# Optimization experiments

Measured on AMD Instinct MI355X. Metric: run time of the kernel, lower is better.

## Reference

```python
import jax, jax.numpy as jnp
import numpy as np

D_MODEL = 1024
HEADS = 16
D_KEY = D_MODEL // HEADS


def setup_inputs() -> dict:
    key = jax.random.key(0)
    ks = jax.random.split(key, 7)
    B, S = 4, 2048
    queries = jax.random.normal(ks[0], (B, S, D_MODEL), dtype=jnp.float32)
    keys = jax.random.normal(ks[1], (B, S, D_MODEL), dtype=jnp.float32)
    values = jax.random.normal(ks[2], (B, S, D_MODEL), dtype=jnp.float32)
    scale = 1.0 / np.sqrt(D_MODEL)
    # Per-head projection weights, torch Linear layout [out=d_key, in=d_model], stacked over heads
    Wq = jax.random.uniform(ks[3], (HEADS, D_KEY, D_MODEL), jnp.float32, -scale, scale)
    Wk = jax.random.uniform(ks[4], (HEADS, D_KEY, D_MODEL), jnp.float32, -scale, scale)
    Wv = jax.random.uniform(ks[5], (HEADS, D_KEY, D_MODEL), jnp.float32, -scale, scale)
    Wo = jax.random.uniform(ks[6], (D_MODEL, D_MODEL), jnp.float32, -scale, scale)
    return {"queries": queries, "keys": keys, "values": values,
            "Wq": Wq, "Wk": Wk, "Wv": Wv, "Wo": Wo}


def reference(queries, keys, values, Wq, Wk, Wv, Wo):
    # Project per head: [B,S,D] x [H,K,D] -> [B,H,S,K]
    q = jnp.einsum('bsd,hkd->bhsk', queries, Wq)
    k = jnp.einsum('bsd,hkd->bhsk', keys, Wk)
    v = jnp.einsum('bsd,hkd->bhsk', values, Wv)
    attn = jnp.einsum('bhqk,bhsk->bhqs', q, k) / jnp.sqrt(jnp.float32(D_KEY))
    attn = jax.nn.softmax(attn, axis=-1)
    out = jnp.einsum('bhqs,bhsk->bhqk', attn, v)  # [B,H,S,K]
    B, H, S, K = out.shape
    # concat heads along last dim (head order = torch cat order)
    out = out.transpose(0, 2, 1, 3).reshape(B, S, H * K)
    return out @ Wo.T
```

## Files before the change

### kernel.cpp

```cpp
#include <hip/hip_runtime.h>
#include <hip/hip_bf16.h>

typedef __attribute__((ext_vector_type(8))) short short8;
typedef __attribute__((ext_vector_type(4))) short short4v;
typedef __attribute__((ext_vector_type(4))) float f32x4;
typedef __bf16 bf16x8 __attribute__((ext_vector_type(8)));
typedef __attribute__((ext_vector_type(2))) unsigned int u32x2;
typedef __attribute__((ext_vector_type(4))) unsigned int u32x4;

#define DEVI static __device__ __forceinline__

DEVI short f2bs(float f) {
    union { __hip_bfloat16 h; short s; } u;
    u.h = __float2bfloat16(f);
    return u.s;
}

DEVI unsigned pack2(float a, float b) {
    union { short s[2]; unsigned u; } u;
    u.s[0] = f2bs(a);
    u.s[1] = f2bs(b);
    return u.u;
}

DEVI void xchg(unsigned& x, unsigned& y) {
#if __has_builtin(__builtin_amdgcn_permlane32_swap) && __has_builtin(__builtin_amdgcn_permlane16_swap)
    u32x2 t = __builtin_amdgcn_permlane32_swap(x, y, false, false);
    u32x2 r = __builtin_amdgcn_permlane16_swap(t[0], t[1], false, false);
    x = r[0];
    y = r[1];
#else
    asm("v_permlane32_swap_b32 %0, %1" : "+v"(x), "+v"(y));
    asm("v_permlane16_swap_b32 %0, %1" : "+v"(x), "+v"(y));
#endif
}

DEVI f32x4 mfma16(short8 a, short8 b, f32x4 c) {
    return __builtin_amdgcn_mfma_f32_16x16x32_bf16(
        __builtin_bit_cast(bf16x8, a), __builtin_bit_cast(bf16x8, b), c, 0, 0, 0);
}

DEVI void glds16(const short* g, short* l) {
    __builtin_amdgcn_global_load_lds((const __attribute__((address_space(1))) void*)g,
                                     (__attribute__((address_space(3))) void*)l, 16, 0, 0);
}

__global__ __launch_bounds__(256) void cvt_all(const float4* __restrict__ q,
                                               const float4* __restrict__ k,
                                               const float4* __restrict__ v,
                                               const float4* __restrict__ wq,
                                               const float4* __restrict__ wk,
                                               const float4* __restrict__ wv,
                                               const float4* __restrict__ wo,
                                               short4v* __restrict__ dq,
                                               short4v* __restrict__ dk,
                                               short4v* __restrict__ dv,
                                               short4v* __restrict__ dwq,
                                               short4v* __restrict__ dwk,
                                               short4v* __restrict__ dwv,
                                               short4v* __restrict__ dwo) {
    int bid = blockIdx.x;
    float4 x;
    short4v s;
    if (bid < 8192) {
        int i = bid * 256 + threadIdx.x;
        x = q[i]; s.x = f2bs(x.x); s.y = f2bs(x.y); s.z = f2bs(x.z); s.w = f2bs(x.w); dq[i] = s;
        x = k[i]; s.x = f2bs(x.x); s.y = f2bs(x.y); s.z = f2bs(x.z); s.w = f2bs(x.w); dk[i] = s;
        x = v[i]; s.x = f2bs(x.x); s.y = f2bs(x.y); s.z = f2bs(x.z); s.w = f2bs(x.w); dv[i] = s;
    } else {
        int i = (bid - 8192) * 256 + threadIdx.x;
        x = wq[i]; s.x = f2bs(x.x); s.y = f2bs(x.y); s.z = f2bs(x.z); s.w = f2bs(x.w); dwq[i] = s;
        x = wk[i]; s.x = f2bs(x.x); s.y = f2bs(x.y); s.z = f2bs(x.z); s.w = f2bs(x.w); dwk[i] = s;
        x = wv[i]; s.x = f2bs(x.x); s.y = f2bs(x.y); s.z = f2bs(x.z); s.w = f2bs(x.w); dwv[i] = s;
        x = wo[i]; s.x = f2bs(x.x); s.y = f2bs(x.y); s.z = f2bs(x.z); s.w = f2bs(x.w); dwo[i] = s;
    }
}

template <typename EpiT>
DEVI void gemm_body(const short* A, const short* Bw, short* smem, int m0, int n0, EpiT epi) {
    short* As = smem;
    short* Bs = smem + 8192;
    const int t = threadIdx.x;
    const int lane = t & 63, w = t >> 6;
    const int col = lane & 15, quad = lane >> 4;
    const int wm = (w & 1) * 64, wn = (w >> 1) * 64;

    f32x4 acc[4][4];
#pragma unroll
    for (int i = 0; i < 4; ++i)
#pragma unroll
        for (int j = 0; j < 4; ++j) acc[i][j] = (f32x4){0.f, 0.f, 0.f, 0.f};

    for (int kt = 0; kt < 16; ++kt) {
        const int k0 = kt * 64;
#pragma unroll
        for (int j = 0; j < 4; ++j) {
            int cbase = (j * 4 + w) * 64;
            int c = cbase + lane;
            int row = c >> 3, kc = (c & 7) ^ (row & 7);
            glds16(A + (size_t)(m0 + row) * 1024 + k0 + kc * 8, As + cbase * 8);
        }
#pragma unroll
        for (int j = 0; j < 4; ++j) {
            int cbase = (j * 4 + w) * 64;
            int c = cbase + lane;
            int row = c >> 3, kc = (c & 7) ^ (row & 7);
            glds16(Bw + (size_t)(n0 + row) * 1024 + k0 + kc * 8, Bs + cbase * 8);
        }
        __syncthreads();
#pragma unroll
        for (int ks = 0; ks < 2; ++ks) {
            short8 a[4], b[4];
#pragma unroll
            for (int i = 0; i < 4; ++i) {
                int row = wm + i * 16 + col;
                int kc = (ks * 4 + quad) ^ (col & 7);
                a[i] = *(const short8*)(As + (row * 8 + kc) * 8);
            }
#pragma unroll
            for (int i = 0; i < 4; ++i) {
                int row = wn + i * 16 + col;
                int kc = (ks * 4 + quad) ^ (col & 7);
                b[i] = *(const short8*)(Bs + (row * 8 + kc) * 8);
            }
#pragma unroll
            for (int mi = 0; mi < 4; ++mi)
#pragma unroll
                for (int ni = 0; ni < 4; ++ni)
                    acc[mi][ni] = mfma16(a[mi], b[ni], acc[mi][ni]);
        }
        __syncthreads();
    }
    epi(acc, wm, wn, col, quad);
}

__global__ __launch_bounds__(256) void qkv_gemm(const short* __restrict__ xq,
                                                const short* __restrict__ xk,
                                                const short* __restrict__ xv,
                                                const short* __restrict__ wq,
                                                const short* __restrict__ wk,
                                                const short* __restrict__ wv,
                                                short* __restrict__ qp,
                                                short* __restrict__ kp,
                                                short* __restrict__ vpt, float qscale) {
    __shared__ __align__(16) short smem[17408];
    const int z = blockIdx.z;
    const int m0 = blockIdx.y * 128, n0 = blockIdx.x * 128;
    const short* A = (z == 0) ? xq : (z == 1) ? xk : xv;
    const short* W = (z == 0) ? wq : (z == 1) ? wk : wv;

    if (z < 2) {
        short* outs = (z == 0) ? qp : kp;
        const float scale = (z == 0) ? qscale : 1.0f;
        gemm_body(A, W, smem, m0, n0, [&](f32x4 (&acc)[4][4], int wm, int wn, int col, int quad) {
            short* T = smem;
#pragma unroll
            for (int mi = 0; mi < 4; ++mi)
#pragma unroll
                for (int ni = 0; ni < 4; ++ni)
#pragma unroll
                    for (int r = 0; r < 4; ++r)
                        T[(wm + mi * 16 + quad * 4 + r) * 136 + wn + ni * 16 + col] =
                            f2bs(acc[mi][ni][r] * scale);
            __syncthreads();
            int t = threadIdx.x;
            int ml = t >> 1, nh = (t & 1) * 64;
            int m = m0 + ml;
            int b = m >> 11, s = m & 2047;
#pragma unroll
            for (int j = 0; j < 8; ++j) {
                int n = n0 + nh + j * 8;
                short8 vv = *(const short8*)(T + ml * 136 + nh + j * 8);
                size_t off = ((size_t)(b * 16 + (n >> 6)) * 2048 + s) * 64 + (n & 63);
                *(short8*)(outs + off) = vv;
            }
        });
    } else {
        gemm_body(A, W, smem, m0, n0, [&](f32x4 (&acc)[4][4], int wm, int wn, int col, int quad) {
            short* T = smem;
#pragma unroll
            for (int mi = 0; mi < 4; ++mi)
#pragma unroll
                for (int ni = 0; ni < 4; ++ni) {
                    int n_l = wn + ni * 16 + col;
                    int m_l = wm + mi * 16 + quad * 4;
                    short4v sv;
                    sv.x = f2bs(acc[mi][ni][0]); sv.y = f2bs(acc[mi][ni][1]);
                    sv.z = f2bs(acc[mi][ni][2]); sv.w = f2bs(acc[mi][ni][3]);
                    *(short4v*)(T + n_l * 132 + m_l) = sv;
                }
            __syncthreads();
            int t = threadIdx.x;
            int nrow = t >> 1, mh = (t & 1) * 64;
            int b = m0 >> 11, s0 = m0 & 2047;
            size_t base = ((size_t)(b * 1024 + n0 + nrow)) * 2048 + s0 + mh;
#pragma unroll
            for (int j = 0; j < 16; ++j) {
                unsigned long long vv = *(const unsigned long long*)(T + nrow * 132 + mh + j * 4);
                *(unsigned long long*)(vpt + base + j * 4) = vv;
            }
        });
    }
}

__global__ __launch_bounds__(256) void out_gemm(const short* __restrict__ ao,
                                                const short* __restrict__ wo,
                                                float* __restrict__ outf) {
    __shared__ __align__(16) short smem[16896];
    const int m0 = blockIdx.y * 128, n0 = blockIdx.x * 128;
    gemm_body(ao, wo, smem, m0, n0, [&](f32x4 (&acc)[4][4], int wm, int wn, int col, int quad) {
#pragma unroll
        for (int mi = 0; mi < 4; ++mi)
#pragma unroll
            for (int ni = 0; ni < 4; ++ni)
#pragma unroll
                for (int r = 0; r < 4; ++r) {
                    int m = m0 + wm + mi * 16 + quad * 4 + r;
                    int n = n0 + wn + ni * 16 + col;
                    outf[(size_t)m * 1024 + n] = acc[mi][ni][r];
                }
    });
}

__global__ __launch_bounds__(256, 4) void flash_attn(const short* __restrict__ qp,
                                                     const short* __restrict__ kp,
                                                     const short* __restrict__ vpt,
                                                     short* __restrict__ ao) {
    __shared__ __align__(16) short smem[8192 + 8192];
    short* Ks = smem;
    short* Vs = smem + 8192;

    const int t = threadIdx.x, lane = t & 63, w = t >> 6;
    const int col = lane & 15, quad = lane >> 4;
    const int bh = blockIdx.x, q0 = blockIdx.y * 128;
    const short* qb = qp + (size_t)bh * 2048 * 64;
    const short* kb = kp + (size_t)bh * 2048 * 64;
    const short* vb = vpt + (size_t)bh * 64 * 2048;

#pragma unroll
    for (int j = 0; j < 4; ++j) {
        int cbase = (j * 4 + w) * 64;
        int c = cbase + lane;
        int row = c >> 3, kc = (c & 7) ^ (row & 7);
        glds16(qb + (size_t)(q0 + row) * 64 + kc * 8, Ks + cbase * 8);
    }
    __syncthreads();
    short8 bQ[2][2];
#pragma unroll
    for (int qi = 0; qi < 2; ++qi)
#pragma unroll
        for (int ks = 0; ks < 2; ++ks) {
            int row = w * 32 + qi * 16 + col;
            int kc = (ks * 4 + quad) ^ (col & 7);
            bQ[qi][ks] = *(const short8*)(Ks + (row * 8 + kc) * 8);
        }
    __syncthreads();

    f32x4 acc_o[2][4];
    float l_r[2] = {0.f, 0.f};
#pragma unroll
    for (int qi = 0; qi < 2; ++qi)
#pragma unroll
        for (int ni = 0; ni < 4; ++ni) acc_o[qi][ni] = (f32x4){0.f, 0.f, 0.f, 0.f};

    for (int kt = 0; kt < 16; ++kt) {
#pragma unroll
        for (int j = 0; j < 4; ++j) {
            int cbase = (j * 4 + w) * 64;
            int c = cbase + lane;
            int row = c >> 3, kc = (c & 7) ^ (row & 7);
            glds16(kb + (size_t)(kt * 128 + row) * 64 + kc * 8, Ks + cbase * 8);
        }
#pragma unroll
        for (int j = 0; j < 4; ++j) {
            int m = w * 4 + j;
            int dk = m * 4 + (lane >> 4);
            int sc = (lane & 15) ^ (dk & 15);
            glds16(vb + (size_t)dk * 2048 + kt * 128 + sc * 8, Vs + m * 512);
        }
        __syncthreads();

#pragma unroll
        for (int g = 0; g < 4; ++g) {
            unsigned pdw[2][4];
#pragma unroll
            for (int h = 0; h < 2; ++h) {
                int kei = g * 2 + h;
                f32x4 st[2];
                st[0] = (f32x4){0.f, 0.f, 0.f, 0.f};
                st[1] = (f32x4){0.f, 0.f, 0.f, 0.f};
                __builtin_amdgcn_s_setprio(1);
#pragma unroll
                for (int ks = 0; ks < 2; ++ks) {
                    int row = kei * 16 + col;
                    int kc = (ks * 4 + quad) ^ (col & 7);
                    short8 aK = *(const short8*)(Ks + (row * 8 + kc) * 8);
#pragma unroll
                    for (int qi = 0; qi < 2; ++qi) st[qi] = mfma16(aK, bQ[qi][ks], st[qi]);
                }
                __builtin_amdgcn_s_setprio(0);
#pragma unroll
                for (int qi = 0; qi < 2; ++qi) {
                    float p0 = __builtin_amdgcn_exp2f(st[qi][0]);
                    float p1 = __builtin_amdgcn_exp2f(st[qi][1]);
                    float p2 = __builtin_amdgcn_exp2f(st[qi][2]);
                    float p3 = __builtin_amdgcn_exp2f(st[qi][3]);
                    l_r[qi] += (p0 + p1) + (p2 + p3);
                    pdw[qi][h * 2]     = pack2(p0, p1);
                    pdw[qi][h * 2 + 1] = pack2(p2, p3);
                }
            }
            short8 pa[2];
#pragma unroll
            for (int qi = 0; qi < 2; ++qi) {
                xchg(pdw[qi][0], pdw[qi][2]);
                xchg(pdw[qi][1], pdw[qi][3]);
                u32x4 pv = {pdw[qi][0], pdw[qi][1], pdw[qi][2], pdw[qi][3]};
                pa[qi] = __builtin_bit_cast(short8, pv);
            }
            __builtin_amdgcn_s_setprio(1);
#pragma unroll
            for (int ni = 0; ni < 4; ++ni) {
                int dk = ni * 16 + col;
                short8 bv = *(const short8*)(Vs + dk * 128 + (((g * 4 + quad) ^ col) * 8));
#pragma unroll
                for (int qi = 0; qi < 2; ++qi)
                    acc_o[qi][ni] = mfma16(pa[qi], bv, acc_o[qi][ni]);
            }
            __builtin_amdgcn_s_setprio(0);
        }
        __syncthreads();
    }

#pragma unroll
    for (int qi = 0; qi < 2; ++qi) {
        l_r[qi] += __shfl_xor(l_r[qi], 16);
        l_r[qi] += __shfl_xor(l_r[qi], 32);
    }
    const int b = bh >> 4, hd = bh & 15;
#pragma unroll
    for (int qi = 0; qi < 2; ++qi)
#pragma unroll
        for (int r = 0; r < 4; ++r) {
            float lq = __shfl(l_r[qi], quad * 4 + r);
            float inv = 1.0f / lq;
            int q = q0 + w * 32 + qi * 16 + quad * 4 + r;
#pragma unroll
            for (int ni = 0; ni < 4; ++ni)
                ao[((size_t)(b * 2048 + q)) * 1024 + hd * 64 + ni * 16 + col] =
                    f2bs(acc_o[qi][ni][r] * inv);
        }
}

extern "C" void kernel_launch(void* const* d_in, const int* in_sizes, int n_in,
                              void* d_out, int out_size, void* d_ws, size_t ws_size,
                              hipStream_t stream) {
    const float* q  = (const float*)d_in[0];
    const float* k  = (const float*)d_in[1];
    const float* v  = (const float*)d_in[2];
    const float* Wq = (const float*)d_in[3];
    const float* Wk = (const float*)d_in[4];
    const float* Wv = (const float*)d_in[5];
    const float* Wo = (const float*)d_in[6];
    float* out = (float*)d_out;

    short* ws = (short*)d_ws;
    const size_t SZ = (size_t)64 * 2048 * 64;
    const size_t WZ = (size_t)1024 * 1024;
    short* xq  = ws;
    short* xk  = ws + SZ;
    short* xv  = ws + 2 * SZ;
    short* qp  = ws + 3 * SZ;
    short* kp  = ws + 4 * SZ;
    short* wqb = ws + 5 * SZ;
    short* wkb = wqb + WZ;
    short* wvb = wqb + 2 * WZ;
    short* wob = wqb + 3 * WZ;
    short* ao  = xq;
    short* vpt = xk;

    const float QSCALE = 0.125f * 1.44269504088896f;

    cvt_all<<<dim3(9216), dim3(256), 0, stream>>>(
        (const float4*)q, (const float4*)k, (const float4*)v, (const float4*)Wq,
        (const float4*)Wk, (const float4*)Wv, (const float4*)Wo, (short4v*)xq, (short4v*)xk,
        (short4v*)xv, (short4v*)wqb, (short4v*)wkb, (short4v*)wvb, (short4v*)wob);
    dim3 blk(256);
    qkv_gemm<<<dim3(8, 64, 3), blk, 0, stream>>>(xq, xk, xv, wqb, wkb, wvb, qp, kp, vpt, QSCALE);
    flash_attn<<<dim3(64, 16), blk, 0, stream>>>(qp, kp, vpt, ao);
    out_gemm<<<dim3(8, 64), blk, 0, stream>>>(ao, wob, out);
}
```

Measured before the change: 344.0 us.

## Double-buffer K/V tiles in flash attention and compute row sums via MFMA

Splits the key loop into 32 tiles of 64 keys with two LDS buffers, so the next K/V tile's global-to-LDS loads are issued while the current tile is being computed, and each iteration needs one barrier instead of two. It also replaces the scalar row-sum accumulation and the final cross-lane shuffle reduction with an extra MFMA of P against a vector of bf16 ones. The intent is to hide memory latency and trim VALU work, at the cost of two extra MFMAs per group and summing bf16-rounded probabilities instead of fp32 ones.

```diff
diff --git a/kernel.cpp b/kernel.cpp
--- a/kernel.cpp
+++ b/kernel.cpp
@@ -226,9 +226,9 @@
                                                      const short* __restrict__ kp,
                                                      const short* __restrict__ vpt,
                                                      short* __restrict__ ao) {
-    __shared__ __align__(16) short smem[8192 + 8192];
-    short* Ks = smem;
-    short* Vs = smem + 8192;
+    __shared__ __align__(16) short smem[16384];
+    short* Ks2 = smem;
+    short* Vs2 = smem + 8192;
 
     const int t = threadIdx.x, lane = t & 63, w = t >> 6;
     const int col = lane & 15, quad = lane >> 4;
@@ -242,7 +242,7 @@
         int cbase = (j * 4 + w) * 64;
         int c = cbase + lane;
         int row = c >> 3, kc = (c & 7) ^ (row & 7);
-        glds16(qb + (size_t)(q0 + row) * 64 + kc * 8, Ks + cbase * 8);
+        glds16(qb + (size_t)(q0 + row) * 64 + kc * 8, smem + cbase * 8);
     }
     __syncthreads();
     short8 bQ[2][2];
@@ -252,98 +252,122 @@
         for (int ks = 0; ks < 2; ++ks) {
             int row = w * 32 + qi * 16 + col;
             int kc = (ks * 4 + quad) ^ (col & 7);
-            bQ[qi][ks] = *(const short8*)(Ks + (row * 8 + kc) * 8);
+            bQ[qi][ks] = *(const short8*)(smem + (row * 8 + kc) * 8);
         }
     __syncthreads();
 
-    f32x4 acc_o[2][4];
-    float l_r[2] = {0.f, 0.f};
-#pragma unroll
-    for (int qi = 0; qi < 2; ++qi)
+    const int base2_0 = col * 64 + ((quad ^ (col & 7)) * 8);
+    const int base2_1 = col * 64 + (((4 + quad) ^ (col & 7)) * 8);
+
+    const short* kg0;
+    const short* kg1;
+    const short* vg0;
+    const short* vg1;
+    {
+        int c0 = w * 64 + lane, c1 = (4 + w) * 64 + lane;
+        int r0 = c0 >> 3, p0 = c0 & 7, r1 = c1 >> 3, p1 = c1 & 7;
+        kg0 = kb + r0 * 64 + ((p0 ^ (r0 & 7)) * 8);
+        kg1 = kb + r1 * 64 + ((p1 ^ (r1 & 7)) * 8);
+        vg0 = vb + (size_t)r0 * 2048 + ((p0 ^ (r0 & 7)) * 8);
+        vg1 = vb + (size_t)r1 * 2048 + ((p1 ^ (r1 & 7)) * 8);
+    }
+
+    f32x4 acc_o[2][4], acc_l[2];
+#pragma unroll
+    for (int qi = 0; qi < 2; ++qi) {
+        acc_l[qi] = (f32x4){0.f, 0.f, 0.f, 0.f};
 #pragma unroll
         for (int ni = 0; ni < 4; ++ni) acc_o[qi][ni] = (f32x4){0.f, 0.f, 0.f, 0.f};
-
-    for (int kt = 0; kt < 16; ++kt) {
-#pragma unroll
-        for (int j = 0; j < 4; ++j) {
-            int cbase = (j * 4 + w) * 64;
-            int c = cbase + lane;
-            int row = c >> 3, kc = (c & 7) ^ (row & 7);
-            glds16(kb + (size_t)(kt * 128 + row) * 64 + kc * 8, Ks + cbase * 8);
-        }
-#pragma unroll
-        for (int j = 0; j < 4; ++j) {
-            int m = w * 4 + j;
-            int dk = m * 4 + (lane >> 4);
-            int sc = (lane & 15) ^ (dk & 15);
-            glds16(vb + (size_t)dk * 2048 + kt * 128 + sc * 8, Vs + m * 512);
-        }
-        __syncthreads();
-
-#pragma unroll
-        for (int g = 0; g < 4; ++g) {
+    }
+    const short ONE = 0x3F80;
+    const short8 vones = {ONE, ONE, ONE, ONE, ONE, ONE, ONE, ONE};
+
+    glds16(kg0, Ks2 + w * 512);
+    glds16(kg1, Ks2 + (4 + w) * 512);
+    glds16(vg0, Vs2 + w * 512);
+    glds16(vg1, Vs2 + (4 + w) * 512);
+    kg0 += 4096; kg1 += 4096; vg0 += 64; vg1 += 64;
+    __syncthreads();
+
+#pragma unroll 2
+    for (int kt = 0; kt < 32; ++kt) {
+        const int cur = kt & 1;
+        if (kt < 31) {
+            const int nxt = cur ^ 1;
+            glds16(kg0, Ks2 + nxt * 4096 + w * 512);
+            glds16(kg1, Ks2 + nxt * 4096 + (4 + w) * 512);
+            glds16(vg0, Vs2 + nxt * 4096 + w * 512);
+            glds16(vg1, Vs2 + nxt * 4096 + (4 + w) * 512);
+            kg0 += 4096; kg1 += 4096; vg0 += 64; vg1 += 64;
+        }
+        const short* Ks = Ks2 + cur * 4096;
+        const short* Vs = Vs2 + cur * 4096;
+
+#pragma unroll
+        for (int g = 0; g < 2; ++g) {
             unsigned pdw[2][4];
 #pragma unroll
             for (int h = 0; h < 2; ++h) {
-                int kei = g * 2 + h;
-                f32x4 st[2];
-                st[0] = (f32x4){0.f, 0.f, 0.f, 0.f};
-                st[1] = (f32x4){0.f, 0.f, 0.f, 0.f};
+                const int kei = g * 2 + h;
+                f32x4 st0 = (f32x4){0.f, 0.f, 0.f, 0.f};
+                f32x4 st1 = (f32x4){0.f, 0.f, 0.f, 0.f};
                 __builtin_amdgcn_s_setprio(1);
-#pragma unroll
-                for (int ks = 0; ks < 2; ++ks) {
-                    int row = kei * 16 + col;
-                    int kc = (ks * 4 + quad) ^ (col & 7);
-                    short8 aK = *(const short8*)(Ks + (row * 8 + kc) * 8);
-#pragma unroll
-                    for (int qi = 0; qi < 2; ++qi) st[qi] = mfma16(aK, bQ[qi][ks], st[qi]);
+                {
+                    short8 aK0 = *(const short8*)(Ks + base2_0 + kei * 1024);
+                    st0 = mfma16(aK0, bQ[0][0], st0);
+                    st1 = mfma16(aK0, bQ[1][0], st1);
+                    short8 aK1 = *(const short8*)(Ks + base2_1 + kei * 1024);
+                    st0 = mfma16(aK1, bQ[0][1], st0);
+                    st1 = mfma16(aK1, bQ[1][1], st1);
                 }
                 __builtin_amdgcn_s_setprio(0);
-#pragma unroll
-                for (int qi = 0; qi < 2; ++qi) {
-                    float p0 = __builtin_amdgcn_exp2f(st[qi][0]);
-                    float p1 = __builtin_amdgcn_exp2f(st[qi][1]);
-                    float p2 = __builtin_amdgcn_exp2f(st[qi][2]);
-                    float p3 = __builtin_amdgcn_exp2f(st[qi][3]);
-                    l_r[qi] += (p0 + p1) + (p2 + p3);
-                    pdw[qi][h * 2]     = pack2(p0, p1);
-                    pdw[qi][h * 2 + 1] = pack2(p2, p3);
+                {
+                    float p0 = __builtin_amdgcn_exp2f(st0[0]);
+                    float p1 = __builtin_amdgcn_exp2f(st0[1]);
+                    float p2 = __builtin_amdgcn_exp2f(st0[2]);
+                    float p3 = __builtin_amdgcn_exp2f(st0[3]);
+                    pdw[0][h * 2] = pack2(p0, p1);
+                    pdw[0][h * 2 + 1] = pack2(p2, p3);
                 }
-            }
-            short8 pa[2];
-#pragma unroll
-            for (int qi = 0; qi < 2; ++qi) {
-                xchg(pdw[qi][0], pdw[qi][2]);
-                xchg(pdw[qi][1], pdw[qi][3]);
-                u32x4 pv = {pdw[qi][0], pdw[qi][1], pdw[qi][2], pdw[qi][3]};
-                pa[qi] = __builtin_bit_cast(short8, pv);
-            }
+                {
+                    float p0 = __builtin_amdgcn_exp2f(st1[0]);
+                    float p1 = __builtin_amdgcn_exp2f(st1[1]);
+                    float p2 = __builtin_amdgcn_exp2f(st1[2]);
+                    float p3 = __builtin_amdgcn_exp2f(st1[3]);
+                    pdw[1][h * 2] = pack2(p0, p1);
+                    pdw[1][h * 2 + 1] = pack2(p2, p3);
+                }
+            }
+            xchg(pdw[0][0], pdw[0][2]);
+            xchg(pdw[0][1], pdw[0][3]);
+            xchg(pdw[1][0], pdw[1][2]);
+            xchg(pdw[1][1], pdw[1][3]);
+            u32x4 pv0 = {pdw[0][0], pdw[0][1], pdw[0][2], pdw[0][3]};
+            u32x4 pv1 = {pdw[1][0], pdw[1][1], pdw[1][2], pdw[1][3]};
+            short8 pa0 = __builtin_bit_cast(short8, pv0);
+            short8 pa1 = __builtin_bit_cast(short8, pv1);
+
+            const int vb2 = (g == 0) ? base2_0 : base2_1;
             __builtin_amdgcn_s_setprio(1);
 #pragma unroll
             for (int ni = 0; ni < 4; ++ni) {
-                int dk = ni * 16 + col;
-                short8 bv = *(const short8*)(Vs + dk * 128 + (((g * 4 + quad) ^ col) * 8));
-#pragma unroll
-                for (int qi = 0; qi < 2; ++qi)
-                    acc_o[qi][ni] = mfma16(pa[qi], bv, acc_o[qi][ni]);
-            }
+                short8 bv = *(const short8*)(Vs + vb2 + ni * 1024);
+                acc_o[0][ni] = mfma16(pa0, bv, acc_o[0][ni]);
+                acc_o[1][ni] = mfma16(pa1, bv, acc_o[1][ni]);
+            }
+            acc_l[0] = mfma16(pa0, vones, acc_l[0]);
+            acc_l[1] = mfma16(pa1, vones, acc_l[1]);
             __builtin_amdgcn_s_setprio(0);
         }
         __syncthreads();
     }
 
-#pragma unroll
-    for (int qi = 0; qi < 2; ++qi) {
-        l_r[qi] += __shfl_xor(l_r[qi], 16);
-        l_r[qi] += __shfl_xor(l_r[qi], 32);
-    }
     const int b = bh >> 4, hd = bh & 15;
 #pragma unroll
     for (int qi = 0; qi < 2; ++qi)
 #pragma unroll
         for (int r = 0; r < 4; ++r) {
-            float lq = __shfl(l_r[qi], quad * 4 + r);
-            float inv = 1.0f / lq;
+            float inv = 1.0f / acc_l[qi][r];
             int q = q0 + w * 32 + qi * 16 + quad * 4 + r;
 #pragma unroll
             for (int ni = 0; ni < 4; ++ni)
```

Measured after the change: 338.7 us. No clear change (-1.5%).
